# Optimization experiments

Hardware: AMD Instinct MI355X
Metric: run time of the kernel (lower is better)

Reference implementation:

```python
import jax, jax.numpy as jnp
import numpy as np

N = 100000
E = 1600000
NFEAT, NHID, NCLASS = 128, 128, 64


def setup_inputs() -> dict:
    key = jax.random.key(0)
    ks = jax.random.split(key, 8)
    x = jax.random.normal(ks[0], (N, NFEAT), dtype=jnp.float32)
    edge_index = jax.random.randint(ks[1], (2, E), 0, N, dtype=jnp.int32)
    def glorot(k, fan_in, fan_out):
        s = (6.0 / (fan_in + fan_out)) ** 0.5
        return jax.random.uniform(k, (fan_in, fan_out), jnp.float32, -s, s)
    W0 = glorot(ks[2], NFEAT, NHID)
    b0 = jnp.zeros((NHID,), jnp.float32)
    W1 = glorot(ks[3], NHID, NHID)
    b1 = jnp.zeros((NHID,), jnp.float32)
    W2 = glorot(ks[4], NHID, NCLASS)
    b2 = jnp.zeros((NCLASS,), jnp.float32)
    return {"x": x, "edge_index": edge_index, "W0": W0, "b0": b0,
            "W1": W1, "b1": b1, "W2": W2, "b2": b2}


def _normalized_adj(edge_index):
    # add self-loops (SparseTensor.set_diag)
    loops = jnp.arange(N, dtype=edge_index.dtype)
    row = jnp.concatenate([edge_index[0], loops])
    col = jnp.concatenate([edge_index[1], loops])
    ones = jnp.ones(row.shape[0], jnp.float32)
    deg = jax.ops.segment_sum(ones, row, num_segments=N)  # row sums incl. self-loop
    dis = jnp.where(deg > 0, deg ** -0.5, 0.0)
    w = dis[row] * dis[col]  # DAD: D^-1/2 A D^-1/2
    return row, col, w


def _spmm(row, col, w, h):
    # A @ h via gather + segment-sum: [E+N, d] intermediate
    return jax.ops.segment_sum(w[:, None] * h[col], row, num_segments=N)


def reference(x, edge_index, W0, b0, W1, b1, W2, b2):
    row, col, w = _normalized_adj(edge_index)
    h = x
    for Wl, bl, last in ((W0, b0, False), (W1, b1, False), (W2, b2, True)):
        h = _spmm(row, col, w, h @ Wl) + bl  # GCNConv(normalize=False)
        if not last:
            h = jax.nn.relu(h)  # dropout p=0.0 -> identity
    return h
```

## Files before the change

### kernel.cpp

```cpp
#include <hip/hip_runtime.h>


typedef __attribute__((ext_vector_type(8))) short bf16x8;
typedef __attribute__((ext_vector_type(4))) float floatx4;

#define STRIDE 96


__device__ inline unsigned short f2bf(float f) {
    union { float f; unsigned u; } v; v.f = f;
    unsigned r = v.u + 0x7fffu + ((v.u >> 16) & 1u);
    return (unsigned short)(r >> 16);
}

__device__ inline float bf2f(unsigned short h) {
    union { unsigned u; float f; } v; v.u = (unsigned)h << 16;
    return v.f;
}

__device__ inline void split_bf(float v, unsigned short& h, unsigned short& l) {
    h = f2bf(v);
    l = f2bf(v - bf2f(h));
}

__device__ inline void bf2x_to_f(unsigned u, float& a, float& b) {
    union { unsigned x; float f; } lo, hi;
    lo.x = u << 16; hi.x = u & 0xffff0000u;
    a = lo.f; b = hi.f;
}

__device__ inline void accw8(float* acc, uint4 u, float w) {
    float a, b;
    bf2x_to_f(u.x, a, b); acc[0] = fmaf(w, a, acc[0]); acc[1] = fmaf(w, b, acc[1]);
    bf2x_to_f(u.y, a, b); acc[2] = fmaf(w, a, acc[2]); acc[3] = fmaf(w, b, acc[3]);
    bf2x_to_f(u.z, a, b); acc[4] = fmaf(w, a, acc[4]); acc[5] = fmaf(w, b, acc[5]);
    bf2x_to_f(u.w, a, b); acc[6] = fmaf(w, a, acc[6]); acc[7] = fmaf(w, b, acc[7]);
}


__global__ void k_zero(int* __restrict__ slab, int n) {
    int i = blockIdx.x * blockDim.x + threadIdx.x;
    if (i < n) slab[(size_t)i * STRIDE] = 0;
}

__global__ void k_edges(const int* __restrict__ row, const int* __restrict__ col,
                        int* __restrict__ slab, int e) {
    int base = (blockIdx.x * blockDim.x + threadIdx.x) * 8;
    if (base + 7 < e) {
        int4 r0 = *(const int4*)&row[base];
        int4 r1 = *(const int4*)&row[base + 4];
        int4 c0 = *(const int4*)&col[base];
        int4 c1 = *(const int4*)&col[base + 4];
        int s0 = atomicAdd(&slab[(size_t)r0.x * STRIDE], 1);
        int s1 = atomicAdd(&slab[(size_t)r0.y * STRIDE], 1);
        int s2 = atomicAdd(&slab[(size_t)r0.z * STRIDE], 1);
        int s3 = atomicAdd(&slab[(size_t)r0.w * STRIDE], 1);
        int s4 = atomicAdd(&slab[(size_t)r1.x * STRIDE], 1);
        int s5 = atomicAdd(&slab[(size_t)r1.y * STRIDE], 1);
        int s6 = atomicAdd(&slab[(size_t)r1.z * STRIDE], 1);
        int s7 = atomicAdd(&slab[(size_t)r1.w * STRIDE], 1);
        if (s0 < STRIDE - 1) slab[(size_t)r0.x * STRIDE + 1 + s0] = c0.x;
        if (s1 < STRIDE - 1) slab[(size_t)r0.y * STRIDE + 1 + s1] = c0.y;
        if (s2 < STRIDE - 1) slab[(size_t)r0.z * STRIDE + 1 + s2] = c0.z;
        if (s3 < STRIDE - 1) slab[(size_t)r0.w * STRIDE + 1 + s3] = c0.w;
        if (s4 < STRIDE - 1) slab[(size_t)r1.x * STRIDE + 1 + s4] = c1.x;
        if (s5 < STRIDE - 1) slab[(size_t)r1.y * STRIDE + 1 + s5] = c1.y;
        if (s6 < STRIDE - 1) slab[(size_t)r1.z * STRIDE + 1 + s6] = c1.z;
        if (s7 < STRIDE - 1) slab[(size_t)r1.w * STRIDE + 1 + s7] = c1.w;
    } else {
        for (int k = base; k < e; k++) {
            int r = row[k];
            int s = atomicAdd(&slab[(size_t)r * STRIDE], 1);
            if (s < STRIDE - 1) slab[(size_t)r * STRIDE + 1 + s] = col[k];
        }
    }
}

__global__ void k_dis(const int* __restrict__ slab, float* __restrict__ dis, int n) {
    int i = blockIdx.x * blockDim.x + threadIdx.x;
    if (i < n) dis[i] = rsqrtf((float)(slab[(size_t)i * STRIDE] + 1));
}


__global__ void k_prep(const float* __restrict__ X, unsigned short* __restrict__ Xhi,
                       unsigned short* __restrict__ Xlo,
                       const float* __restrict__ W0, const float* __restrict__ W1,
                       const float* __restrict__ W2,
                       unsigned short* __restrict__ Wt0h, unsigned short* __restrict__ Wt0l,
                       unsigned short* __restrict__ Wt1h, unsigned short* __restrict__ Wt1l,
                       unsigned short* __restrict__ Wt2h, unsigned short* __restrict__ Wt2l,
                       int total4) {
    int gid = blockIdx.x * blockDim.x + threadIdx.x;
    int gsz = gridDim.x * blockDim.x;
    for (int id = gid; id < total4; id += gsz) {
        float4 v = ((const float4*)X)[id];
        ushort4 h, l;
        split_bf(v.x, h.x, l.x);
        split_bf(v.y, h.y, l.y);
        split_bf(v.z, h.z, l.z);
        split_bf(v.w, h.w, l.w);
        ((ushort4*)Xhi)[id] = h;
        ((ushort4*)Xlo)[id] = l;
    }
    for (int id = gid; id < 128 * 128; id += gsz) {
        int k = id >> 7, nn = id & 127;
        unsigned short h, l;
        split_bf(W0[id], h, l);
        Wt0h[nn * 128 + k] = h;
        Wt0l[nn * 128 + k] = l;
        split_bf(W1[id], h, l);
        Wt1h[nn * 128 + k] = h;
        Wt1l[nn * 128 + k] = l;
    }
    for (int id = gid; id < 128 * 64; id += gsz) {
        int k = id >> 6, nn = id & 63;
        unsigned short h, l;
        split_bf(W2[id], h, l);
        Wt2h[nn * 128 + k] = h;
        Wt2l[nn * 128 + k] = l;
    }
}


template <int NB>
__global__ __launch_bounds__(256) void k_gemm_mfma(
    const unsigned short* __restrict__ Ahi, const unsigned short* __restrict__ Alo,
    const unsigned short* __restrict__ Wthi, const unsigned short* __restrict__ Wtlo,
    const float* __restrict__ dis, unsigned short* __restrict__ T, int n) {
    const int LDW = NB * 64;
    __shared__ unsigned short Ah_s[64 * 128];
    __shared__ unsigned short Al_s[64 * 128];
    const int tid = threadIdx.x;
    const int bid = blockIdx.x;
    const int bx = (NB == 2) ? (bid >> 1) : bid;
    const int by = (NB == 2) ? (bid & 1) : 0;
    const int row0 = bx * 64;
    const int col0 = by * 64;

    const int wave = tid >> 6, lane = tid & 63;
    const int ln = lane & 15, quad = lane >> 4;
    const int m0 = (wave >> 1) * 32;
    const int nq0 = (wave & 1) * 32;

    bf16x8 Bh[4][2], Bl[4][2];
#pragma unroll
    for (int s = 0; s < 4; s++)
#pragma unroll
        for (int j = 0; j < 2; j++) {
            int ncol = col0 + nq0 + 16 * j + ln;
            int koff = 32 * s + quad * 8;
            Bh[s][j] = *(const bf16x8*)&Wthi[ncol * 128 + koff];
            Bl[s][j] = *(const bf16x8*)&Wtlo[ncol * 128 + koff];
        }

#pragma unroll
    for (int k = 0; k < 4; k++) {
        int id = k * 256 + tid;
        int r = id >> 4, c = id & 15;
        int gr = row0 + r;
        uint4 vh = make_uint4(0, 0, 0, 0), vl = make_uint4(0, 0, 0, 0);
        if (gr < n) {
            vh = *(const uint4*)&Ahi[(size_t)gr * 128 + c * 8];
            vl = *(const uint4*)&Alo[(size_t)gr * 128 + c * 8];
        }
        int pc = c ^ (r & 15);
        *(uint4*)&Ah_s[r * 128 + pc * 8] = vh;
        *(uint4*)&Al_s[r * 128 + pc * 8] = vl;
    }
    __syncthreads();

    floatx4 acc[2][2];
#pragma unroll
    for (int i = 0; i < 2; i++)
#pragma unroll
        for (int j = 0; j < 2; j++) acc[i][j] = (floatx4){0.f, 0.f, 0.f, 0.f};

#pragma unroll
    for (int s = 0; s < 4; s++) {
        bf16x8 ah[2], al[2];
#pragma unroll
        for (int i = 0; i < 2; i++) {
            int off = (m0 + 16 * i + ln) * 128 + ((4 * s + quad) ^ ln) * 8;
            ah[i] = *(const bf16x8*)&Ah_s[off];
            al[i] = *(const bf16x8*)&Al_s[off];
        }
#pragma unroll
        for (int i = 0; i < 2; i++)
#pragma unroll
            for (int j = 0; j < 2; j++) {
                acc[i][j] = __builtin_amdgcn_mfma_f32_16x16x32_bf16(
                    ah[i], Bh[s][j], acc[i][j], 0, 0, 0);
                acc[i][j] = __builtin_amdgcn_mfma_f32_16x16x32_bf16(
                    ah[i], Bl[s][j], acc[i][j], 0, 0, 0);
                acc[i][j] = __builtin_amdgcn_mfma_f32_16x16x32_bf16(
                    al[i], Bh[s][j], acc[i][j], 0, 0, 0);
            }
    }

#pragma unroll
    for (int i = 0; i < 2; i++)
#pragma unroll
        for (int reg = 0; reg < 4; reg++) {
            int gr = row0 + m0 + 16 * i + quad * 4 + reg;
            if (gr < n) {
                float ds = dis[gr];
#pragma unroll
                for (int j = 0; j < 2; j++) {
                    int gc = col0 + nq0 + 16 * j + ln;
                    T[(size_t)gr * LDW + gc] = f2bf(ds * acc[i][j][reg]);
                }
            }
        }
}


__global__ void k_agg128(const unsigned short* __restrict__ T,
                         unsigned short* __restrict__ Ohi,
                         unsigned short* __restrict__ Olo,
                         const int* __restrict__ slab,
                         const float* __restrict__ dis, const float* __restrict__ bias,
                         int n) {
    int wid = (blockIdx.x * blockDim.x + threadIdx.x) >> 6;
    int lane = threadIdx.x & 63;
    if (wid >= n) return;
    const int quad = lane >> 4;
    const int fl = (lane & 15) * 8;
    int beg = wid * STRIDE + 1;
    int deg = slab[(size_t)wid * STRIDE];
    if (deg > STRIDE - 1) deg = STRIDE - 1;
    int end = beg + deg;
    int span = (deg + 3) >> 2;
    int qb = beg + quad * span;
    int qe = qb + span;
    if (qe > end) qe = end;

    float acc[8] = {0.f, 0.f, 0.f, 0.f, 0.f, 0.f, 0.f, 0.f};
    for (int e = qb; e < qe; e += 4) {
        int l = qe - 1;
        int i1 = e + 1, i2 = e + 2, i3 = e + 3;
        int c0 = slab[e];
        int c1 = slab[i1 < l ? i1 : l];
        int c2 = slab[i2 < l ? i2 : l];
        int c3 = slab[i3 < l ? i3 : l];
        float m1 = (i1 < qe) ? 1.f : 0.f;
        float m2 = (i2 < qe) ? 1.f : 0.f;
        float m3 = (i3 < qe) ? 1.f : 0.f;
        uint4 u0 = *(const uint4*)&T[(size_t)c0 * 128 + fl];
        uint4 u1 = *(const uint4*)&T[(size_t)c1 * 128 + fl];
        uint4 u2 = *(const uint4*)&T[(size_t)c2 * 128 + fl];
        uint4 u3 = *(const uint4*)&T[(size_t)c3 * 128 + fl];
        accw8(acc, u0, 1.f);
        accw8(acc, u1, m1);
        accw8(acc, u2, m2);
        accw8(acc, u3, m3);
    }
#pragma unroll
    for (int k = 0; k < 8; k++) {
        acc[k] += __shfl_xor(acc[k], 16);
        acc[k] += __shfl_xor(acc[k], 32);
    }
    if (quad == 0) {
        uint4 us = *(const uint4*)&T[(size_t)wid * 128 + fl];
        accw8(acc, us, 1.f);
        float di = dis[wid];
        float4 bA = *(const float4*)&bias[fl];
        float4 bB = *(const float4*)&bias[fl + 4];
        float bb[8] = {bA.x, bA.y, bA.z, bA.w, bB.x, bB.y, bB.z, bB.w};
        unsigned short h[8], l[8];
#pragma unroll
        for (int k = 0; k < 8; k++) {
            float o = fmaf(di, acc[k], bb[k]);
            o = fmaxf(o, 0.f);
            split_bf(o, h[k], l[k]);
        }
        ushort4 h0 = {h[0], h[1], h[2], h[3]}, h1 = {h[4], h[5], h[6], h[7]};
        ushort4 l0 = {l[0], l[1], l[2], l[3]}, l1 = {l[4], l[5], l[6], l[7]};
        *(ushort4*)&Ohi[(size_t)wid * 128 + fl] = h0;
        *(ushort4*)&Ohi[(size_t)wid * 128 + fl + 4] = h1;
        *(ushort4*)&Olo[(size_t)wid * 128 + fl] = l0;
        *(ushort4*)&Olo[(size_t)wid * 128 + fl + 4] = l1;
    }
}

__global__ void k_agg64(const unsigned short* __restrict__ T, float* __restrict__ O,
                        const int* __restrict__ slab,
                        const float* __restrict__ dis, const float* __restrict__ bias,
                        int n) {
    int wid = (blockIdx.x * blockDim.x + threadIdx.x) >> 6;
    int lane = threadIdx.x & 63;
    if (wid >= n) return;
    const int oct = lane >> 3;
    const int fl = (lane & 7) * 8;
    int beg = wid * STRIDE + 1;
    int deg = slab[(size_t)wid * STRIDE];
    if (deg > STRIDE - 1) deg = STRIDE - 1;
    int end = beg + deg;
    int span = (deg + 7) >> 3;
    int qb = beg + oct * span;
    int qe = qb + span;
    if (qe > end) qe = end;

    float acc[8] = {0.f, 0.f, 0.f, 0.f, 0.f, 0.f, 0.f, 0.f};
    for (int e = qb; e < qe; e += 4) {
        int l = qe - 1;
        int i1 = e + 1, i2 = e + 2, i3 = e + 3;
        int c0 = slab[e];
        int c1 = slab[i1 < l ? i1 : l];
        int c2 = slab[i2 < l ? i2 : l];
        int c3 = slab[i3 < l ? i3 : l];
        float m1 = (i1 < qe) ? 1.f : 0.f;
        float m2 = (i2 < qe) ? 1.f : 0.f;
        float m3 = (i3 < qe) ? 1.f : 0.f;
        uint4 u0 = *(const uint4*)&T[(size_t)c0 * 64 + fl];
        uint4 u1 = *(const uint4*)&T[(size_t)c1 * 64 + fl];
        uint4 u2 = *(const uint4*)&T[(size_t)c2 * 64 + fl];
        uint4 u3 = *(const uint4*)&T[(size_t)c3 * 64 + fl];
        accw8(acc, u0, 1.f);
        accw8(acc, u1, m1);
        accw8(acc, u2, m2);
        accw8(acc, u3, m3);
    }
#pragma unroll
    for (int k = 0; k < 8; k++) {
        acc[k] += __shfl_xor(acc[k], 8);
        acc[k] += __shfl_xor(acc[k], 16);
        acc[k] += __shfl_xor(acc[k], 32);
    }
    if (oct == 0) {
        uint4 us = *(const uint4*)&T[(size_t)wid * 64 + fl];
        accw8(acc, us, 1.f);
        float di = dis[wid];
        float4 bA = *(const float4*)&bias[fl];
        float4 bB = *(const float4*)&bias[fl + 4];
        float bb[8] = {bA.x, bA.y, bA.z, bA.w, bB.x, bB.y, bB.z, bB.w};
        float o[8];
#pragma unroll
        for (int k = 0; k < 8; k++)
            o[k] = fmaf(di, acc[k], bb[k]);
        *(float4*)&O[(size_t)wid * 64 + fl] = make_float4(o[0], o[1], o[2], o[3]);
        *(float4*)&O[(size_t)wid * 64 + fl + 4] = make_float4(o[4], o[5], o[6], o[7]);
    }
}


static inline char* align256(char* p) {
    return (char*)(((uintptr_t)p + 255) & ~(uintptr_t)255);
}

extern "C" void kernel_launch(void* const* d_in, const int* in_sizes, int n_in,
                              void* d_out, int out_size, void* d_ws, size_t ws_size,
                              hipStream_t stream) {
    const float* x  = (const float*)d_in[0];
    const int*   ei = (const int*)d_in[1];
    const float* W0 = (const float*)d_in[2];
    const float* b0 = (const float*)d_in[3];
    const float* W1 = (const float*)d_in[4];
    const float* b1 = (const float*)d_in[5];
    const float* W2 = (const float*)d_in[6];
    const float* b2 = (const float*)d_in[7];

    const int Nn = in_sizes[0] / 128;
    const int Ee = in_sizes[1] / 2;
    const int* rowI = ei;
    const int* colI = ei + Ee;

    char* p = (char*)d_ws;
    unsigned short* Tb  = (unsigned short*)p; p += (size_t)Nn * 128 * 2; p = align256(p);
    unsigned short* Ahi = (unsigned short*)p; p += (size_t)Nn * 128 * 2; p = align256(p);
    unsigned short* Alo = (unsigned short*)p; p += (size_t)Nn * 128 * 2; p = align256(p);
    int* slab   = (int*)p;   p += (size_t)Nn * STRIDE * 4; p = align256(p);
    float* dis  = (float*)p; p += (size_t)Nn * 4;          p = align256(p);
    unsigned short* Wt0h = (unsigned short*)p; p += 128 * 128 * 2;
    unsigned short* Wt0l = (unsigned short*)p; p += 128 * 128 * 2;
    unsigned short* Wt1h = (unsigned short*)p; p += 128 * 128 * 2;
    unsigned short* Wt1l = (unsigned short*)p; p += 128 * 128 * 2;
    unsigned short* Wt2h = (unsigned short*)p; p += 64 * 128 * 2;
    unsigned short* Wt2l = (unsigned short*)p; p += 64 * 128 * 2;

    const int nb = (Nn + 255) / 256;
    const int eb8 = (Ee / 8 + 255) / 256;

    k_zero<<<nb, 256, 0, stream>>>(slab, Nn);
    k_edges<<<eb8, 256, 0, stream>>>(rowI, colI, slab, Ee);
    k_dis<<<nb, 256, 0, stream>>>(slab, dis, Nn);
    k_prep<<<512, 256, 0, stream>>>(x, Ahi, Alo, W0, W1, W2,
                                    Wt0h, Wt0l, Wt1h, Wt1l, Wt2h, Wt2l, Nn * 32);

    const int gx = (Nn + 63) / 64;
    const int ab = (Nn + 3) / 4;

    k_gemm_mfma<2><<<2 * gx, 256, 0, stream>>>(Ahi, Alo, Wt0h, Wt0l, dis, Tb, Nn);
    k_agg128<<<ab, 256, 0, stream>>>(Tb, Ahi, Alo, slab, dis, b0, Nn);
    k_gemm_mfma<2><<<2 * gx, 256, 0, stream>>>(Ahi, Alo, Wt1h, Wt1l, dis, Tb, Nn);
    k_agg128<<<ab, 256, 0, stream>>>(Tb, Ahi, Alo, slab, dis, b1, Nn);
    k_gemm_mfma<1><<<gx, 256, 0, stream>>>(Ahi, Alo, Wt2h, Wt2l, dis, Tb, Nn);
    k_agg64<<<ab, 256, 0, stream>>>(Tb, (float*)d_out, slab, dis, b2, Nn);
}
```

Baseline: 469.6 us.

## Store hidden features in 16-column slices and aggregate per slice for cache locality

The GEMM now writes its 128-wide bf16 output as eight column slices of 16 features each, laid out contiguously per slice. A new aggregation kernel gives each block one slice and a range of nodes, so the gathered working set per slice (about 3.2 MB) can stay in cache while neighbor indices are read with nontemporal loads. The separate zero and degree-normalisation kernels are removed: zeroing moves into the prep kernel, and rsqrt of the degree is recomputed inline from the slab. In exchange, each adjacency list is read eight times, once per slice, and each gather moves only 4 bytes per lane.

```diff
diff --git a/kernel.cpp b/kernel.cpp
--- a/kernel.cpp
+++ b/kernel.cpp
@@ -37,11 +37,8 @@
     bf2x_to_f(u.w, a, b); acc[6] = fmaf(w, a, acc[6]); acc[7] = fmaf(w, b, acc[7]);
 }
 
-
-__global__ void k_zero(int* __restrict__ slab, int n) {
-    int i = blockIdx.x * blockDim.x + threadIdx.x;
-    if (i < n) slab[(size_t)i * STRIDE] = 0;
-}
+__device__ inline int ntl(const int* p) { return __builtin_nontemporal_load(p); }
+
 
 __global__ void k_edges(const int* __restrict__ row, const int* __restrict__ col,
                         int* __restrict__ slab, int e) {
@@ -76,11 +73,6 @@
     }
 }
 
-__global__ void k_dis(const int* __restrict__ slab, float* __restrict__ dis, int n) {
-    int i = blockIdx.x * blockDim.x + threadIdx.x;
-    if (i < n) dis[i] = rsqrtf((float)(slab[(size_t)i * STRIDE] + 1));
-}
-
 
 __global__ void k_prep(const float* __restrict__ X, unsigned short* __restrict__ Xhi,
                        unsigned short* __restrict__ Xlo,
@@ -89,9 +81,10 @@
                        unsigned short* __restrict__ Wt0h, unsigned short* __restrict__ Wt0l,
                        unsigned short* __restrict__ Wt1h, unsigned short* __restrict__ Wt1l,
                        unsigned short* __restrict__ Wt2h, unsigned short* __restrict__ Wt2l,
-                       int total4) {
+                       int* __restrict__ slab, int n, int total4) {
     int gid = blockIdx.x * blockDim.x + threadIdx.x;
     int gsz = gridDim.x * blockDim.x;
+    for (int i = gid; i < n; i += gsz) slab[(size_t)i * STRIDE] = 0;
     for (int id = gid; id < total4; id += gsz) {
         float4 v = ((const float4*)X)[id];
         ushort4 h, l;
@@ -122,11 +115,11 @@
 }
 
 
-template <int NB>
+template <int NB, bool SLICED>
 __global__ __launch_bounds__(256) void k_gemm_mfma(
     const unsigned short* __restrict__ Ahi, const unsigned short* __restrict__ Alo,
     const unsigned short* __restrict__ Wthi, const unsigned short* __restrict__ Wtlo,
-    const float* __restrict__ dis, unsigned short* __restrict__ T, int n) {
+    const int* __restrict__ slab, unsigned short* __restrict__ T, int n) {
     const int LDW = NB * 64;
     __shared__ unsigned short Ah_s[64 * 128];
     __shared__ unsigned short Al_s[64 * 128];
@@ -203,88 +196,84 @@
         for (int reg = 0; reg < 4; reg++) {
             int gr = row0 + m0 + 16 * i + quad * 4 + reg;
             if (gr < n) {
-                float ds = dis[gr];
+                int degt = slab[(size_t)gr * STRIDE];
+                float ds = rsqrtf((float)(degt + 1));
 #pragma unroll
                 for (int j = 0; j < 2; j++) {
-                    int gc = col0 + nq0 + 16 * j + ln;
-                    T[(size_t)gr * LDW + gc] = f2bf(ds * acc[i][j][reg]);
+                    unsigned short o = f2bf(ds * acc[i][j][reg]);
+                    if (SLICED) {
+                        int s = ((col0 + nq0) >> 4) + j;
+                        T[((size_t)s * n + gr) * 16 + ln] = o;
+                    } else {
+                        int gc = col0 + nq0 + 16 * j + ln;
+                        T[(size_t)gr * LDW + gc] = o;
+                    }
                 }
             }
         }
 }
 
 
-__global__ void k_agg128(const unsigned short* __restrict__ T,
-                         unsigned short* __restrict__ Ohi,
-                         unsigned short* __restrict__ Olo,
-                         const int* __restrict__ slab,
-                         const float* __restrict__ dis, const float* __restrict__ bias,
-                         int n) {
-    int wid = (blockIdx.x * blockDim.x + threadIdx.x) >> 6;
-    int lane = threadIdx.x & 63;
-    if (wid >= n) return;
-    const int quad = lane >> 4;
-    const int fl = (lane & 15) * 8;
-    int beg = wid * STRIDE + 1;
-    int deg = slab[(size_t)wid * STRIDE];
-    if (deg > STRIDE - 1) deg = STRIDE - 1;
-    int end = beg + deg;
-    int span = (deg + 3) >> 2;
-    int qb = beg + quad * span;
-    int qe = qb + span;
-    if (qe > end) qe = end;
-
-    float acc[8] = {0.f, 0.f, 0.f, 0.f, 0.f, 0.f, 0.f, 0.f};
-    for (int e = qb; e < qe; e += 4) {
-        int l = qe - 1;
-        int i1 = e + 1, i2 = e + 2, i3 = e + 3;
-        int c0 = slab[e];
-        int c1 = slab[i1 < l ? i1 : l];
-        int c2 = slab[i2 < l ? i2 : l];
-        int c3 = slab[i3 < l ? i3 : l];
-        float m1 = (i1 < qe) ? 1.f : 0.f;
-        float m2 = (i2 < qe) ? 1.f : 0.f;
-        float m3 = (i3 < qe) ? 1.f : 0.f;
-        uint4 u0 = *(const uint4*)&T[(size_t)c0 * 128 + fl];
-        uint4 u1 = *(const uint4*)&T[(size_t)c1 * 128 + fl];
-        uint4 u2 = *(const uint4*)&T[(size_t)c2 * 128 + fl];
-        uint4 u3 = *(const uint4*)&T[(size_t)c3 * 128 + fl];
-        accw8(acc, u0, 1.f);
-        accw8(acc, u1, m1);
-        accw8(acc, u2, m2);
-        accw8(acc, u3, m3);
-    }
-#pragma unroll
-    for (int k = 0; k < 8; k++) {
-        acc[k] += __shfl_xor(acc[k], 16);
-        acc[k] += __shfl_xor(acc[k], 32);
-    }
-    if (quad == 0) {
-        uint4 us = *(const uint4*)&T[(size_t)wid * 128 + fl];
-        accw8(acc, us, 1.f);
-        float di = dis[wid];
-        float4 bA = *(const float4*)&bias[fl];
-        float4 bB = *(const float4*)&bias[fl + 4];
-        float bb[8] = {bA.x, bA.y, bA.z, bA.w, bB.x, bB.y, bB.z, bB.w};
-        unsigned short h[8], l[8];
-#pragma unroll
-        for (int k = 0; k < 8; k++) {
-            float o = fmaf(di, acc[k], bb[k]);
-            o = fmaxf(o, 0.f);
-            split_bf(o, h[k], l[k]);
-        }
-        ushort4 h0 = {h[0], h[1], h[2], h[3]}, h1 = {h[4], h[5], h[6], h[7]};
-        ushort4 l0 = {l[0], l[1], l[2], l[3]}, l1 = {l[4], l[5], l[6], l[7]};
-        *(ushort4*)&Ohi[(size_t)wid * 128 + fl] = h0;
-        *(ushort4*)&Ohi[(size_t)wid * 128 + fl + 4] = h1;
-        *(ushort4*)&Olo[(size_t)wid * 128 + fl] = l0;
-        *(ushort4*)&Olo[(size_t)wid * 128 + fl + 4] = l1;
-    }
-}
+__global__ __launch_bounds__(256) void k_agg128s(
+    const unsigned short* __restrict__ Ts,
+    unsigned short* __restrict__ Ohi, unsigned short* __restrict__ Olo,
+    const int* __restrict__ slab, const float* __restrict__ bias,
+    int n, int npb) {
+    const int s = blockIdx.x & 7;
+    const int nb0 = (blockIdx.x >> 3) * npb;
+    const int wave = threadIdx.x >> 6, lane = threadIdx.x & 63;
+    const int g = lane >> 3;
+    const int fo = lane & 7;
+    const unsigned short* Tsl = Ts + (size_t)s * n * 16;
+    int nend = nb0 + npb;
+    if (nend > n) nend = n;
+
+    for (int wid = nb0 + wave; wid < nend; wid += 4) {
+        const int* sl = slab + (size_t)wid * STRIDE;
+        int degt = ntl(sl);
+        int deg = (degt > STRIDE - 1) ? (STRIDE - 1) : degt;
+        float a0 = 0.f, a1 = 0.f;
+        int e = g;
+        for (; e + 8 < deg; e += 16) {
+            int c0 = ntl(&sl[1 + e]);
+            int c1 = ntl(&sl[1 + e + 8]);
+            unsigned u0 = *(const unsigned*)&Tsl[(size_t)c0 * 16 + fo * 2];
+            unsigned u1 = *(const unsigned*)&Tsl[(size_t)c1 * 16 + fo * 2];
+            float x, y;
+            bf2x_to_f(u0, x, y); a0 += x; a1 += y;
+            bf2x_to_f(u1, x, y); a0 += x; a1 += y;
+        }
+        if (e < deg) {
+            int c0 = ntl(&sl[1 + e]);
+            unsigned u0 = *(const unsigned*)&Tsl[(size_t)c0 * 16 + fo * 2];
+            float x, y;
+            bf2x_to_f(u0, x, y); a0 += x; a1 += y;
+        }
+        a0 += __shfl_xor(a0, 8);  a1 += __shfl_xor(a1, 8);
+        a0 += __shfl_xor(a0, 16); a1 += __shfl_xor(a1, 16);
+        a0 += __shfl_xor(a0, 32); a1 += __shfl_xor(a1, 32);
+        if (g == 0) {
+            unsigned us = *(const unsigned*)&Tsl[(size_t)wid * 16 + fo * 2];
+            float sx, sy;
+            bf2x_to_f(us, sx, sy);
+            a0 += sx; a1 += sy;
+            float di = rsqrtf((float)(degt + 1));
+            float2 bb = *(const float2*)&bias[s * 16 + fo * 2];
+            float o0 = fmaxf(fmaf(di, a0, bb.x), 0.f);
+            float o1 = fmaxf(fmaf(di, a1, bb.y), 0.f);
+            unsigned short h0, l0, h1, l1;
+            split_bf(o0, h0, l0);
+            split_bf(o1, h1, l1);
+            size_t ob = (size_t)wid * 128 + s * 16 + fo * 2;
+            *(unsigned*)&Ohi[ob] = (unsigned)h0 | ((unsigned)h1 << 16);
+            *(unsigned*)&Olo[ob] = (unsigned)l0 | ((unsigned)l1 << 16);
+        }
+    }
+}
+
 
 __global__ void k_agg64(const unsigned short* __restrict__ T, float* __restrict__ O,
-                        const int* __restrict__ slab,
-                        const float* __restrict__ dis, const float* __restrict__ bias,
+                        const int* __restrict__ slab, const float* __restrict__ bias,
                         int n) {
     int wid = (blockIdx.x * blockDim.x + threadIdx.x) >> 6;
     int lane = threadIdx.x & 63;
@@ -292,8 +281,8 @@
     const int oct = lane >> 3;
     const int fl = (lane & 7) * 8;
     int beg = wid * STRIDE + 1;
-    int deg = slab[(size_t)wid * STRIDE];
-    if (deg > STRIDE - 1) deg = STRIDE - 1;
+    int degt = slab[(size_t)wid * STRIDE];
+    int deg = (degt > STRIDE - 1) ? (STRIDE - 1) : degt;
     int end = beg + deg;
     int span = (deg + 7) >> 3;
     int qb = beg + oct * span;
@@ -329,7 +318,7 @@
     if (oct == 0) {
         uint4 us = *(const uint4*)&T[(size_t)wid * 64 + fl];
         accw8(acc, us, 1.f);
-        float di = dis[wid];
+        float di = rsqrtf((float)(degt + 1));
         float4 bA = *(const float4*)&bias[fl];
         float4 bB = *(const float4*)&bias[fl + 4];
         float bb[8] = {bA.x, bA.y, bA.z, bA.w, bB.x, bB.y, bB.z, bB.w};
@@ -369,7 +358,6 @@
     unsigned short* Ahi = (unsigned short*)p; p += (size_t)Nn * 128 * 2; p = align256(p);
     unsigned short* Alo = (unsigned short*)p; p += (size_t)Nn * 128 * 2; p = align256(p);
     int* slab   = (int*)p;   p += (size_t)Nn * STRIDE * 4; p = align256(p);
-    float* dis  = (float*)p; p += (size_t)Nn * 4;          p = align256(p);
     unsigned short* Wt0h = (unsigned short*)p; p += 128 * 128 * 2;
     unsigned short* Wt0l = (unsigned short*)p; p += 128 * 128 * 2;
     unsigned short* Wt1h = (unsigned short*)p; p += 128 * 128 * 2;
@@ -377,22 +365,23 @@
     unsigned short* Wt2h = (unsigned short*)p; p += 64 * 128 * 2;
     unsigned short* Wt2l = (unsigned short*)p; p += 64 * 128 * 2;
 
-    const int nb = (Nn + 255) / 256;
     const int eb8 = (Ee / 8 + 255) / 256;
 
-    k_zero<<<nb, 256, 0, stream>>>(slab, Nn);
+    k_prep<<<512, 256, 0, stream>>>(x, Ahi, Alo, W0, W1, W2,
+                                    Wt0h, Wt0l, Wt1h, Wt1l, Wt2h, Wt2l,
+                                    slab, Nn, Nn * 32);
     k_edges<<<eb8, 256, 0, stream>>>(rowI, colI, slab, Ee);
-    k_dis<<<nb, 256, 0, stream>>>(slab, dis, Nn);
-    k_prep<<<512, 256, 0, stream>>>(x, Ahi, Alo, W0, W1, W2,
-                                    Wt0h, Wt0l, Wt1h, Wt1l, Wt2h, Wt2l, Nn * 32);
 
     const int gx = (Nn + 63) / 64;
     const int ab = (Nn + 3) / 4;
-
-    k_gemm_mfma<2><<<2 * gx, 256, 0, stream>>>(Ahi, Alo, Wt0h, Wt0l, dis, Tb, Nn);
-    k_agg128<<<ab, 256, 0, stream>>>(Tb, Ahi, Alo, slab, dis, b0, Nn);
-    k_gemm_mfma<2><<<2 * gx, 256, 0, stream>>>(Ahi, Alo, Wt1h, Wt1l, dis, Tb, Nn);
-    k_agg128<<<ab, 256, 0, stream>>>(Tb, Ahi, Alo, slab, dis, b1, Nn);
-    k_gemm_mfma<1><<<gx, 256, 0, stream>>>(Ahi, Alo, Wt2h, Wt2l, dis, Tb, Nn);
-    k_agg64<<<ab, 256, 0, stream>>>(Tb, (float*)d_out, slab, dis, b2, Nn);
-}
+    const int SB = 256;
+    const int npb = (Nn + SB - 1) / SB;
+    const int ag = SB * 8;
+
+    k_gemm_mfma<2, true><<<2 * gx, 256, 0, stream>>>(Ahi, Alo, Wt0h, Wt0l, slab, Tb, Nn);
+    k_agg128s<<<ag, 256, 0, stream>>>(Tb, Ahi, Alo, slab, b0, Nn, npb);
+    k_gemm_mfma<2, true><<<2 * gx, 256, 0, stream>>>(Ahi, Alo, Wt1h, Wt1l, slab, Tb, Nn);
+    k_agg128s<<<ag, 256, 0, stream>>>(Tb, Ahi, Alo, slab, b1, Nn, npb);
+    k_gemm_mfma<1, false><<<gx, 256, 0, stream>>>(Ahi, Alo, Wt2h, Wt2l, slab, Tb, Nn);
+    k_agg64<<<ab, 256, 0, stream>>>(Tb, (float*)d_out, slab, b2, Nn);
+}
```

New measurement: 957.6 us. 2.04x slower.

## Fuse graph build with input prep, split counts from slab, compute dis inline

Applied to the files above, without the earlier changes.

Merges the edge-bucketing kernel and the bf16 split/transpose prep kernel into one launch, with separate block ranges for each job, so the two independent jobs overlap. Degree counts move to a dense cnt array that is zeroed with a memset, replacing the strided zero kernel. The dis kernel is removed and rsqrt(deg+1) is recomputed wherever it is needed. This cuts three launches and the strided count accesses, at the cost of recomputing rsqrt in the GEMM and aggregation kernels.

```diff
diff --git a/kernel.cpp b/kernel.cpp
--- a/kernel.cpp
+++ b/kernel.cpp
@@ -4,7 +4,8 @@
 typedef __attribute__((ext_vector_type(8))) short bf16x8;
 typedef __attribute__((ext_vector_type(4))) float floatx4;
 
-#define STRIDE 96
+#define SLOTS 96
+#define PB 512
 
 
 __device__ inline unsigned short f2bf(float f) {
@@ -38,86 +39,78 @@
 }
 
 
-__global__ void k_zero(int* __restrict__ slab, int n) {
-    int i = blockIdx.x * blockDim.x + threadIdx.x;
-    if (i < n) slab[(size_t)i * STRIDE] = 0;
-}
-
-__global__ void k_edges(const int* __restrict__ row, const int* __restrict__ col,
-                        int* __restrict__ slab, int e) {
-    int base = (blockIdx.x * blockDim.x + threadIdx.x) * 8;
-    if (base + 7 < e) {
-        int4 r0 = *(const int4*)&row[base];
-        int4 r1 = *(const int4*)&row[base + 4];
-        int4 c0 = *(const int4*)&col[base];
-        int4 c1 = *(const int4*)&col[base + 4];
-        int s0 = atomicAdd(&slab[(size_t)r0.x * STRIDE], 1);
-        int s1 = atomicAdd(&slab[(size_t)r0.y * STRIDE], 1);
-        int s2 = atomicAdd(&slab[(size_t)r0.z * STRIDE], 1);
-        int s3 = atomicAdd(&slab[(size_t)r0.w * STRIDE], 1);
-        int s4 = atomicAdd(&slab[(size_t)r1.x * STRIDE], 1);
-        int s5 = atomicAdd(&slab[(size_t)r1.y * STRIDE], 1);
-        int s6 = atomicAdd(&slab[(size_t)r1.z * STRIDE], 1);
-        int s7 = atomicAdd(&slab[(size_t)r1.w * STRIDE], 1);
-        if (s0 < STRIDE - 1) slab[(size_t)r0.x * STRIDE + 1 + s0] = c0.x;
-        if (s1 < STRIDE - 1) slab[(size_t)r0.y * STRIDE + 1 + s1] = c0.y;
-        if (s2 < STRIDE - 1) slab[(size_t)r0.z * STRIDE + 1 + s2] = c0.z;
-        if (s3 < STRIDE - 1) slab[(size_t)r0.w * STRIDE + 1 + s3] = c0.w;
-        if (s4 < STRIDE - 1) slab[(size_t)r1.x * STRIDE + 1 + s4] = c1.x;
-        if (s5 < STRIDE - 1) slab[(size_t)r1.y * STRIDE + 1 + s5] = c1.y;
-        if (s6 < STRIDE - 1) slab[(size_t)r1.z * STRIDE + 1 + s6] = c1.z;
-        if (s7 < STRIDE - 1) slab[(size_t)r1.w * STRIDE + 1 + s7] = c1.w;
+__global__ __launch_bounds__(256) void k_build(
+    const int* __restrict__ row, const int* __restrict__ col,
+    int* __restrict__ cnt, int* __restrict__ slab,
+    const float* __restrict__ X,
+    unsigned short* __restrict__ Xhi, unsigned short* __restrict__ Xlo,
+    const float* __restrict__ W0, const float* __restrict__ W1,
+    const float* __restrict__ W2,
+    unsigned short* __restrict__ Wt0h, unsigned short* __restrict__ Wt0l,
+    unsigned short* __restrict__ Wt1h, unsigned short* __restrict__ Wt1l,
+    unsigned short* __restrict__ Wt2h, unsigned short* __restrict__ Wt2l,
+    int e, int total4) {
+    const int tid = threadIdx.x;
+    if (blockIdx.x < PB) {
+        int gid = blockIdx.x * 256 + tid;
+        const int gsz = PB * 256;
+        for (int id = gid; id < total4; id += gsz) {
+            float4 v = ((const float4*)X)[id];
+            ushort4 h, l;
+            split_bf(v.x, h.x, l.x);
+            split_bf(v.y, h.y, l.y);
+            split_bf(v.z, h.z, l.z);
+            split_bf(v.w, h.w, l.w);
+            ((ushort4*)Xhi)[id] = h;
+            ((ushort4*)Xlo)[id] = l;
+        }
+        for (int id = gid; id < 128 * 128; id += gsz) {
+            int k = id >> 7, nn = id & 127;
+            unsigned short h, l;
+            split_bf(W0[id], h, l);
+            Wt0h[nn * 128 + k] = h;
+            Wt0l[nn * 128 + k] = l;
+            split_bf(W1[id], h, l);
+            Wt1h[nn * 128 + k] = h;
+            Wt1l[nn * 128 + k] = l;
+        }
+        for (int id = gid; id < 128 * 64; id += gsz) {
+            int k = id >> 6, nn = id & 63;
+            unsigned short h, l;
+            split_bf(W2[id], h, l);
+            Wt2h[nn * 128 + k] = h;
+            Wt2l[nn * 128 + k] = l;
+        }
     } else {
-        for (int k = base; k < e; k++) {
-            int r = row[k];
-            int s = atomicAdd(&slab[(size_t)r * STRIDE], 1);
-            if (s < STRIDE - 1) slab[(size_t)r * STRIDE + 1 + s] = col[k];
-        }
-    }
-}
-
-__global__ void k_dis(const int* __restrict__ slab, float* __restrict__ dis, int n) {
-    int i = blockIdx.x * blockDim.x + threadIdx.x;
-    if (i < n) dis[i] = rsqrtf((float)(slab[(size_t)i * STRIDE] + 1));
-}
-
-
-__global__ void k_prep(const float* __restrict__ X, unsigned short* __restrict__ Xhi,
-                       unsigned short* __restrict__ Xlo,
-                       const float* __restrict__ W0, const float* __restrict__ W1,
-                       const float* __restrict__ W2,
-                       unsigned short* __restrict__ Wt0h, unsigned short* __restrict__ Wt0l,
-                       unsigned short* __restrict__ Wt1h, unsigned short* __restrict__ Wt1l,
-                       unsigned short* __restrict__ Wt2h, unsigned short* __restrict__ Wt2l,
-                       int total4) {
-    int gid = blockIdx.x * blockDim.x + threadIdx.x;
-    int gsz = gridDim.x * blockDim.x;
-    for (int id = gid; id < total4; id += gsz) {
-        float4 v = ((const float4*)X)[id];
-        ushort4 h, l;
-        split_bf(v.x, h.x, l.x);
-        split_bf(v.y, h.y, l.y);
-        split_bf(v.z, h.z, l.z);
-        split_bf(v.w, h.w, l.w);
-        ((ushort4*)Xhi)[id] = h;
-        ((ushort4*)Xlo)[id] = l;
-    }
-    for (int id = gid; id < 128 * 128; id += gsz) {
-        int k = id >> 7, nn = id & 127;
-        unsigned short h, l;
-        split_bf(W0[id], h, l);
-        Wt0h[nn * 128 + k] = h;
-        Wt0l[nn * 128 + k] = l;
-        split_bf(W1[id], h, l);
-        Wt1h[nn * 128 + k] = h;
-        Wt1l[nn * 128 + k] = l;
-    }
-    for (int id = gid; id < 128 * 64; id += gsz) {
-        int k = id >> 6, nn = id & 63;
-        unsigned short h, l;
-        split_bf(W2[id], h, l);
-        Wt2h[nn * 128 + k] = h;
-        Wt2l[nn * 128 + k] = l;
+        int base = ((blockIdx.x - PB) * 256 + tid) * 8;
+        if (base + 7 < e) {
+            int4 r0 = *(const int4*)&row[base];
+            int4 r1 = *(const int4*)&row[base + 4];
+            int4 c0 = *(const int4*)&col[base];
+            int4 c1 = *(const int4*)&col[base + 4];
+            int s0 = atomicAdd(&cnt[r0.x], 1);
+            int s1 = atomicAdd(&cnt[r0.y], 1);
+            int s2 = atomicAdd(&cnt[r0.z], 1);
+            int s3 = atomicAdd(&cnt[r0.w], 1);
+            int s4 = atomicAdd(&cnt[r1.x], 1);
+            int s5 = atomicAdd(&cnt[r1.y], 1);
+            int s6 = atomicAdd(&cnt[r1.z], 1);
+            int s7 = atomicAdd(&cnt[r1.w], 1);
+            if (s0 < SLOTS) slab[(size_t)r0.x * SLOTS + s0] = c0.x;
+            if (s1 < SLOTS) slab[(size_t)r0.y * SLOTS + s1] = c0.y;
+            if (s2 < SLOTS) slab[(size_t)r0.z * SLOTS + s2] = c0.z;
+            if (s3 < SLOTS) slab[(size_t)r0.w * SLOTS + s3] = c0.w;
+            if (s4 < SLOTS) slab[(size_t)r1.x * SLOTS + s4] = c1.x;
+            if (s5 < SLOTS) slab[(size_t)r1.y * SLOTS + s5] = c1.y;
+            if (s6 < SLOTS) slab[(size_t)r1.z * SLOTS + s6] = c1.z;
+            if (s7 < SLOTS) slab[(size_t)r1.w * SLOTS + s7] = c1.w;
+        } else {
+            for (int k = base; k < e; k++) {
+                int r = row[k];
+                int s = atomicAdd(&cnt[r], 1);
+                if (s < SLOTS) slab[(size_t)r * SLOTS + s] = col[k];
+            }
+        }
     }
 }
 
@@ -126,7 +119,7 @@
 __global__ __launch_bounds__(256) void k_gemm_mfma(
     const unsigned short* __restrict__ Ahi, const unsigned short* __restrict__ Alo,
     const unsigned short* __restrict__ Wthi, const unsigned short* __restrict__ Wtlo,
-    const float* __restrict__ dis, unsigned short* __restrict__ T, int n) {
+    const int* __restrict__ cnt, unsigned short* __restrict__ T, int n) {
     const int LDW = NB * 64;
     __shared__ unsigned short Ah_s[64 * 128];
     __shared__ unsigned short Al_s[64 * 128];
@@ -203,7 +196,7 @@
         for (int reg = 0; reg < 4; reg++) {
             int gr = row0 + m0 + 16 * i + quad * 4 + reg;
             if (gr < n) {
-                float ds = dis[gr];
+                float ds = rsqrtf((float)(cnt[gr] + 1));
 #pragma unroll
                 for (int j = 0; j < 2; j++) {
                     int gc = col0 + nq0 + 16 * j + ln;
@@ -217,17 +210,16 @@
 __global__ void k_agg128(const unsigned short* __restrict__ T,
                          unsigned short* __restrict__ Ohi,
                          unsigned short* __restrict__ Olo,
-                         const int* __restrict__ slab,
-                         const float* __restrict__ dis, const float* __restrict__ bias,
-                         int n) {
+                         const int* __restrict__ cnt, const int* __restrict__ slab,
+                         const float* __restrict__ bias, int n) {
     int wid = (blockIdx.x * blockDim.x + threadIdx.x) >> 6;
     int lane = threadIdx.x & 63;
     if (wid >= n) return;
     const int quad = lane >> 4;
     const int fl = (lane & 15) * 8;
-    int beg = wid * STRIDE + 1;
-    int deg = slab[(size_t)wid * STRIDE];
-    if (deg > STRIDE - 1) deg = STRIDE - 1;
+    int degt = cnt[wid];
+    int deg = (degt > SLOTS) ? SLOTS : degt;
+    int beg = wid * SLOTS;
     int end = beg + deg;
     int span = (deg + 3) >> 2;
     int qb = beg + quad * span;
@@ -262,7 +254,7 @@
     if (quad == 0) {
         uint4 us = *(const uint4*)&T[(size_t)wid * 128 + fl];
         accw8(acc, us, 1.f);
-        float di = dis[wid];
+        float di = rsqrtf((float)(degt + 1));
         float4 bA = *(const float4*)&bias[fl];
         float4 bB = *(const float4*)&bias[fl + 4];
         float bb[8] = {bA.x, bA.y, bA.z, bA.w, bB.x, bB.y, bB.z, bB.w};
@@ -283,17 +275,16 @@
 }
 
 __global__ void k_agg64(const unsigned short* __restrict__ T, float* __restrict__ O,
-                        const int* __restrict__ slab,
-                        const float* __restrict__ dis, const float* __restrict__ bias,
-                        int n) {
+                        const int* __restrict__ cnt, const int* __restrict__ slab,
+                        const float* __restrict__ bias, int n) {
     int wid = (blockIdx.x * blockDim.x + threadIdx.x) >> 6;
     int lane = threadIdx.x & 63;
     if (wid >= n) return;
     const int oct = lane >> 3;
     const int fl = (lane & 7) * 8;
-    int beg = wid * STRIDE + 1;
-    int deg = slab[(size_t)wid * STRIDE];
-    if (deg > STRIDE - 1) deg = STRIDE - 1;
+    int degt = cnt[wid];
+    int deg = (degt > SLOTS) ? SLOTS : degt;
+    int beg = wid * SLOTS;
     int end = beg + deg;
     int span = (deg + 7) >> 3;
     int qb = beg + oct * span;
@@ -329,7 +320,7 @@
     if (oct == 0) {
         uint4 us = *(const uint4*)&T[(size_t)wid * 64 + fl];
         accw8(acc, us, 1.f);
-        float di = dis[wid];
+        float di = rsqrtf((float)(degt + 1));
         float4 bA = *(const float4*)&bias[fl];
         float4 bB = *(const float4*)&bias[fl + 4];
         float bb[8] = {bA.x, bA.y, bA.z, bA.w, bB.x, bB.y, bB.z, bB.w};
@@ -368,8 +359,8 @@
     unsigned short* Tb  = (unsigned short*)p; p += (size_t)Nn * 128 * 2; p = align256(p);
     unsigned short* Ahi = (unsigned short*)p; p += (size_t)Nn * 128 * 2; p = align256(p);
     unsigned short* Alo = (unsigned short*)p; p += (size_t)Nn * 128 * 2; p = align256(p);
-    int* slab   = (int*)p;   p += (size_t)Nn * STRIDE * 4; p = align256(p);
-    float* dis  = (float*)p; p += (size_t)Nn * 4;          p = align256(p);
+    int* cnt    = (int*)p;   p += (size_t)Nn * 4;         p = align256(p);
+    int* slab   = (int*)p;   p += (size_t)Nn * SLOTS * 4; p = align256(p);
     unsigned short* Wt0h = (unsigned short*)p; p += 128 * 128 * 2;
     unsigned short* Wt0l = (unsigned short*)p; p += 128 * 128 * 2;
     unsigned short* Wt1h = (unsigned short*)p; p += 128 * 128 * 2;
@@ -377,22 +368,20 @@
     unsigned short* Wt2h = (unsigned short*)p; p += 64 * 128 * 2;
     unsigned short* Wt2l = (unsigned short*)p; p += 64 * 128 * 2;
 
-    const int nb = (Nn + 255) / 256;
     const int eb8 = (Ee / 8 + 255) / 256;
 
-    k_zero<<<nb, 256, 0, stream>>>(slab, Nn);
-    k_edges<<<eb8, 256, 0, stream>>>(rowI, colI, slab, Ee);
-    k_dis<<<nb, 256, 0, stream>>>(slab, dis, Nn);
-    k_prep<<<512, 256, 0, stream>>>(x, Ahi, Alo, W0, W1, W2,
-                                    Wt0h, Wt0l, Wt1h, Wt1l, Wt2h, Wt2l, Nn * 32);
+    hipMemsetAsync(cnt, 0, (size_t)Nn * 4, stream);
+    k_build<<<PB + eb8, 256, 0, stream>>>(rowI, colI, cnt, slab, x, Ahi, Alo,
+                                          W0, W1, W2, Wt0h, Wt0l, Wt1h, Wt1l,
+                                          Wt2h, Wt2l, Ee, Nn * 32);
 
     const int gx = (Nn + 63) / 64;
     const int ab = (Nn + 3) / 4;
 
-    k_gemm_mfma<2><<<2 * gx, 256, 0, stream>>>(Ahi, Alo, Wt0h, Wt0l, dis, Tb, Nn);
-    k_agg128<<<ab, 256, 0, stream>>>(Tb, Ahi, Alo, slab, dis, b0, Nn);
-    k_gemm_mfma<2><<<2 * gx, 256, 0, stream>>>(Ahi, Alo, Wt1h, Wt1l, dis, Tb, Nn);
-    k_agg128<<<ab, 256, 0, stream>>>(Tb, Ahi, Alo, slab, dis, b1, Nn);
-    k_gemm_mfma<1><<<gx, 256, 0, stream>>>(Ahi, Alo, Wt2h, Wt2l, dis, Tb, Nn);
-    k_agg64<<<ab, 256, 0, stream>>>(Tb, (float*)d_out, slab, dis, b2, Nn);
-}
+    k_gemm_mfma<2><<<2 * gx, 256, 0, stream>>>(Ahi, Alo, Wt0h, Wt0l, cnt, Tb, Nn);
+    k_agg128<<<ab, 256, 0, stream>>>(Tb, Ahi, Alo, cnt, slab, b0, Nn);
+    k_gemm_mfma<2><<<2 * gx, 256, 0, stream>>>(Ahi, Alo, Wt1h, Wt1l, cnt, Tb, Nn);
+    k_agg128<<<ab, 256, 0, stream>>>(Tb, Ahi, Alo, cnt, slab, b1, Nn);
+    k_gemm_mfma<1><<<gx, 256, 0, stream>>>(Ahi, Alo, Wt2h, Wt2l, cnt, Tb, Nn);
+    k_agg64<<<ab, 256, 0, stream>>>(Tb, (float*)d_out, cnt, slab, b2, Nn);
+}
```

Measured after the change: 469.7 us. Within noise of the previous version (+0.0%).
